# Kernel optimization log

Hardware: AMD Instinct MI355X
Metric: run time of the kernel (lower is better)

Reference implementation:

```python
import jax, jax.numpy as jnp
import numpy as np

B, L, D_MODEL = 8, 2048, 768
D_INNER, D_STATE, DT_RANK, K = 1536, 16, 48, 4


def setup_inputs() -> dict:
    key = jax.random.key(0)
    ks = jax.random.split(key, 9)
    s = 0.02
    return {
        "hidden_states": jax.random.normal(ks[0], (B, L, D_MODEL), jnp.float32),
        "W_in": jax.random.normal(ks[1], (D_MODEL, 2 * D_INNER), jnp.float32) * s,
        "conv_w": jax.random.normal(ks[2], (D_INNER, 1, K), jnp.float32) * s,
        "conv_b": jax.random.normal(ks[3], (D_INNER,), jnp.float32) * s,
        "W_x": jax.random.normal(ks[4], (DT_RANK + 2 * D_STATE, D_INNER), jnp.float32) * s,
        "W_dt": jax.random.normal(ks[5], (D_INNER, DT_RANK), jnp.float32) * s,
        "b_dt": jax.random.normal(ks[6], (D_INNER,), jnp.float32) * s,
        "A_log": jax.random.normal(ks[7], (D_INNER, D_STATE), jnp.float32),
        "D_param": jax.random.normal(ks[8], (D_INNER,), jnp.float32),
    }


def _mamba(hidden_states, W_in, conv_w, conv_b, W_x, W_dt, b_dt, A_log, D_param):
    # in_proj then chunk into ssm branch (x) and gating residual (res)
    xz = hidden_states @ W_in                      # (B, L, 2*d_inner)
    x, res = jnp.split(xz, 2, axis=-1)             # each (B, L, d_inner)

    # causal depthwise conv over time, then SiLU
    xc = x.transpose(0, 2, 1)                      # (B, C, L)
    xc = jax.lax.conv_general_dilated(
        xc, conv_w, window_strides=(1,), padding=[(K - 1, 0)],
        feature_group_count=D_INNER, dimension_numbers=("NCH", "OIH", "NCH"))
    x = jax.nn.silu(xc + conv_b[None, :, None]).transpose(0, 2, 1)  # (B, L, d_inner)

    # input-dependent SSM parameters
    x_dbl = x @ W_x.T                              # (B, L, dt_rank + 2*d_state)
    dt = jax.nn.softplus(x_dbl[..., :DT_RANK] @ W_dt.T + b_dt)      # (B, L, d_inner)
    Bm = x_dbl[..., DT_RANK:DT_RANK + D_STATE]     # (B, L, d_state)
    Cm = x_dbl[..., DT_RANK + D_STATE:]            # (B, L, d_state)
    A = -jnp.exp(A_log)                            # (d_inner, d_state)

    def step(h, inp):
        x_t, dt_t, B_t, C_t = inp                  # (B,d_inner),(B,d_inner),(B,d_state),(B,d_state)
        dA = jnp.exp(dt_t[..., None] * A)          # (B, d_inner, d_state)
        dBx = (dt_t * x_t)[..., None] * B_t[:, None, :]
        h = dA * h + dBx
        y = jnp.einsum("bds,bs->bd", h, C_t)
        return h, y

    xs = (x.transpose(1, 0, 2), dt.transpose(1, 0, 2),
          Bm.transpose(1, 0, 2), Cm.transpose(1, 0, 2))
    h0 = jnp.zeros((x.shape[0], D_INNER, D_STATE), x.dtype)
    _, ys = jax.lax.scan(step, h0, xs)             # ys: (L, B, d_inner)
    y = ys.transpose(1, 0, 2) + x * D_param        # skip term
    return y * jax.nn.silu(res)                    # gated output (B, L, d_inner)


def reference(hidden_states, W_in, conv_w, conv_b, W_x, W_dt, b_dt, A_log, D_param):
    return _mamba(hidden_states, W_in, conv_w, conv_b, W_x, W_dt, b_dt, A_log, D_param)
```

## Files before the change

kernel.cpp:

```cpp
#include <hip/hip_runtime.h>
#include <hip/hip_bf16.h>
#include <stdint.h>

#define B_SZ 8
#define L_SZ 2048
#define DM 768
#define DI 1536
#define DS 16
#define DR 48
#define M_SZ (B_SZ * L_SZ)
#define N1 (2 * DI)

#define NC 32
#define TC (L_SZ / NC)
#define CH (B_SZ * DI)
#define KS 6
#define NT (DM / 64)
#define L2E 1.44269504088896f

typedef short short8 __attribute__((ext_vector_type(8)));
typedef float f32x4 __attribute__((ext_vector_type(4)));

__device__ __forceinline__ ushort f2b(float f) {
  __hip_bfloat16 h = __float2bfloat16(f);
  return *reinterpret_cast<ushort*>(&h);
}
__device__ __forceinline__ float b2f(ushort u) {
  __hip_bfloat16 h;
  *reinterpret_cast<ushort*>(&h) = u;
  return __bfloat162float(h);
}
__device__ __forceinline__ ushort f2h(float f) {
  _Float16 h = (_Float16)f;
  return *reinterpret_cast<ushort*>(&h);
}
__device__ __forceinline__ float h2f(ushort u) {
  _Float16 h;
  *reinterpret_cast<ushort*>(&h) = u;
  return (float)h;
}

__device__ __forceinline__ void gl16(const ushort* g, ushort* l) {
  __builtin_amdgcn_global_load_lds(
      (const __attribute__((address_space(1))) void*)g,
      (__attribute__((address_space(3))) void*)l, 16, 0, 0);
}

#define EXP4(dst, src)                                      \
  {                                                         \
    float _e0, _e1, _e2, _e3;                               \
    asm("v_exp_f32 %0, %1" : "=v"(_e0) : "v"((src)[0]));    \
    asm("v_exp_f32 %0, %1" : "=v"(_e1) : "v"((src)[1]));    \
    asm("v_exp_f32 %0, %1" : "=v"(_e2) : "v"((src)[2]));    \
    asm("v_exp_f32 %0, %1" : "=v"(_e3) : "v"((src)[3]));    \
    (dst) = f32x4{_e0, _e1, _e2, _e3};                      \
  }


__global__ __launch_bounds__(256) void prep_all(const float4* __restrict__ hs4,
                                                const float* __restrict__ w_in,
                                                const float* __restrict__ wx_f,
                                                const float* __restrict__ wdt_f,
                                                ushort4* __restrict__ A1,
                                                ushort* __restrict__ wt,
                                                ushort* __restrict__ wx_b,
                                                ushort* __restrict__ wdt_p) {
  const int n4 = M_SZ * DM / 4;
  const int nT = 3072 * 96;
  const int nwx = 80 * DI;
  const int nwdt = DI * 64;
  int idx = blockIdx.x * 256 + threadIdx.x;
  if (idx < n4) {
    float4 v = hs4[idx];
    ushort4 o;
    o.x = f2b(v.x); o.y = f2b(v.y); o.z = f2b(v.z); o.w = f2b(v.w);
    A1[idx] = o;
  } else if (idx < n4 + nT) {
    int j = idx - n4;
    int n = j % 3072;
    int kb = (j / 3072) * 8;
    short8 o;
#pragma unroll
    for (int q = 0; q < 8; ++q) o[q] = (short)f2b(w_in[(size_t)(kb + q) * 3072 + n]);
    *(short8*)(wt + (size_t)n * DM + kb) = o;
  } else if (idx < n4 + nT + nwx) {
    int j = idx - n4 - nT;
    wx_b[j] = f2b(wx_f[j]);
  } else if (idx < n4 + nT + nwx + nwdt) {
    int j = idx - n4 - nT - nwx;
    int col = j >> 6, k = j & 63;
    wdt_p[j] = (k < DR) ? f2b(wdt_f[col * DR + k]) : (ushort)0;
  }
}


__global__ __launch_bounds__(512, 1) void gemm_xz(const ushort* __restrict__ A,
                                                  const ushort* __restrict__ Bt,
                                                  ushort* __restrict__ xout,
                                                  ushort* __restrict__ gateout) {
  __shared__ ushort lds[65536];

  const int t = threadIdx.x;
  const int lane = t & 63;
  const int wid = t >> 6;
  const int wm = wid >> 2, wn = wid & 3;
  const int r = lane & 15, hi = lane >> 4;

  const int g = blockIdx.x;
  const int swz = (g & 7) * (768 / 8) + (g >> 3);
  const int bx = swz & 63;
  const int by = swz >> 6;
  const int bm = bx * 256;
  const int bn = by * 256;

  const bool isA = wid < 4;
  const int w4 = wid & 3;
  const ushort* gsrc[8];
  int ldso[8];
#pragma unroll
  for (int i = 0; i < 8; ++i) {
    int c = w4 * 8 + i;
    int mg = c >> 1, kkc = c & 1;
    gsrc[i] = (isA ? A + (size_t)(bm + mg * 16 + r) * DM
                   : Bt + (size_t)(bn + mg * 16 + r) * DM) + kkc * 32 + hi * 8;
    ldso[i] = (isA ? 0 : 16384) + c * 512;
  }

  f32x4 acc[8][4];
#pragma unroll
  for (int m = 0; m < 8; ++m)
#pragma unroll
    for (int n = 0; n < 4; ++n) acc[m][n] = f32x4{0.f, 0.f, 0.f, 0.f};

#pragma unroll
  for (int i = 0; i < 8; ++i) gl16(gsrc[i], &lds[ldso[i]]);
  asm volatile("s_waitcnt vmcnt(0)" ::: "memory");
  __builtin_amdgcn_s_barrier();

  for (int kt = 0; kt < NT; ++kt) {
    const int cur = kt & 1;
    const ushort* bufA = &lds[cur * 32768];
    const ushort* bufB = bufA + 16384;
    ushort* nxt = &lds[(cur ^ 1) * 32768];
    const int koff = (kt + 1) * 64;
    const bool more = (kt + 1 < NT);

    short8 afr[4][2], bfr[2][2];
#pragma unroll
    for (int q = 0; q < 4; ++q) {
      const int mq = q >> 1, nq = q & 1;
      if (nq == 0) {
#pragma unroll
        for (int m = 0; m < 4; ++m)
#pragma unroll
          for (int kk = 0; kk < 2; ++kk)
            afr[m][kk] = *(const short8*)&bufA[((wm * 8 + mq * 4 + m) * 2 + kk) * 512 + lane * 8];
      }
#pragma unroll
      for (int n = 0; n < 2; ++n)
#pragma unroll
        for (int kk = 0; kk < 2; ++kk)
          bfr[n][kk] = *(const short8*)&bufB[((wn * 4 + nq * 2 + n) * 2 + kk) * 512 + lane * 8];

      if (q == 0 && more) {
#pragma unroll
        for (int i = 0; i < 8; ++i) gl16(gsrc[i] + koff, nxt + ldso[i]);
      }

      asm volatile("s_barrier" ::: "memory");

      __builtin_amdgcn_s_setprio(1);
#pragma unroll
      for (int m = 0; m < 4; ++m)
#pragma unroll
        for (int n = 0; n < 2; ++n) {
          f32x4 a = acc[mq * 4 + m][nq * 2 + n];
          a = __builtin_amdgcn_mfma_f32_16x16x32_bf16(afr[m][0], bfr[n][0], a, 0, 0, 0);
          a = __builtin_amdgcn_mfma_f32_16x16x32_bf16(afr[m][1], bfr[n][1], a, 0, 0, 0);
          acc[mq * 4 + m][nq * 2 + n] = a;
        }
      __builtin_amdgcn_s_setprio(0);

      if (q == 3) asm volatile("s_waitcnt vmcnt(0)" ::: "memory");
      asm volatile("s_barrier" ::: "memory");
    }
  }

  const bool isx = (bn < DI);
  ushort* outp = isx ? xout : gateout;
  const int cbase = bn - (isx ? 0 : DI) + wn * 64;
#pragma unroll
  for (int mf = 0; mf < 8; ++mf)
#pragma unroll
    for (int nf = 0; nf < 4; ++nf) {
      int col = cbase + nf * 16 + r;
#pragma unroll
      for (int j = 0; j < 4; ++j) {
        int row = bm + wm * 128 + mf * 16 + hi * 4 + j;
        float v = acc[mf][nf][j];
        if (!isx) v = v / (1.f + __expf(-v));
        outp[(size_t)row * DI + col] = f2b(v);
      }
    }
}


__global__ __launch_bounds__(256) void conv_silu(const ushort* __restrict__ xp,
                                                 const float* __restrict__ cw,
                                                 const float* __restrict__ cb,
                                                 ushort* __restrict__ xc) {
  int tid = blockIdx.x * 256 + threadIdx.x;
  const int nd = DI / 8;
  int db = tid % nd;
  int row = tid / nd;
  int d0 = db * 8;
  int l = row & (L_SZ - 1);
  const ushort* base = xp + (size_t)row * DI + d0;
  short8 z8 = {0, 0, 0, 0, 0, 0, 0, 0};
  short8 x0 = *(const short8*)base;
  short8 xm1 = (l >= 1) ? *(const short8*)(base - DI) : z8;
  short8 xm2 = (l >= 2) ? *(const short8*)(base - 2 * DI) : z8;
  short8 xm3 = (l >= 3) ? *(const short8*)(base - 3 * DI) : z8;
  short8 o;
#pragma unroll
  for (int j = 0; j < 8; ++j) {
    float4 w = *(const float4*)(cw + (size_t)(d0 + j) * 4);
    float a = cb[d0 + j] + w.x * b2f((ushort)xm3[j]) + w.y * b2f((ushort)xm2[j]) +
              w.z * b2f((ushort)xm1[j]) + w.w * b2f((ushort)x0[j]);
    float s = a / (1.f + __expf(-a));
    o[j] = (short)f2b(s);
  }
  *(short8*)(xc + (size_t)row * DI + d0) = o;
}


__global__ __launch_bounds__(256) void xdbl_gemm(const ushort* __restrict__ xc,
                                                 const ushort* __restrict__ wx,
                                                 float* __restrict__ xdp) {
  int wave = blockIdx.x * 4 + (threadIdx.x >> 6);
  int ks = blockIdx.y;
  int lane = threadIdx.x & 63;
  int r = lane & 15, hi = lane >> 4;
  int row0 = wave * 16;
  f32x4 acc[5];
#pragma unroll
  for (int n = 0; n < 5; ++n) acc[n] = f32x4{0.f, 0.f, 0.f, 0.f};
  const int kbeg = ks * (DI / KS), kend = kbeg + DI / KS;
  for (int k0 = kbeg; k0 < kend; k0 += 32) {
    short8 a = *(const short8*)(xc + (size_t)(row0 + r) * DI + k0 + hi * 8);
#pragma unroll
    for (int n = 0; n < 5; ++n) {
      short8 b = *(const short8*)(wx + (size_t)(n * 16 + r) * DI + k0 + hi * 8);
      acc[n] = __builtin_amdgcn_mfma_f32_16x16x32_bf16(a, b, acc[n], 0, 0, 0);
    }
  }
  float* op = xdp + (size_t)ks * M_SZ * 80;
#pragma unroll
  for (int n = 0; n < 5; ++n)
#pragma unroll
    for (int j = 0; j < 4; ++j)
      op[(size_t)(row0 + hi * 4 + j) * 80 + n * 16 + r] = acc[n][j];
}

__global__ __launch_bounds__(256) void reduce_xd(const float4* __restrict__ xdp,
                                                 float4* __restrict__ xd) {
  int i = blockIdx.x * 256 + threadIdx.x;
  if (i >= M_SZ * 20) return;
  float4 s = xdp[i];
#pragma unroll
  for (int k = 1; k < KS; ++k) {
    float4 v = xdp[(size_t)k * M_SZ * 20 + i];
    s.x += v.x; s.y += v.y; s.z += v.z; s.w += v.w;
  }
  xd[i] = s;
}


__device__ __forceinline__ short8 pack8f(const float* p) {
  short8 v;
#pragma unroll
  for (int i = 0; i < 8; ++i) v[i] = (short)f2b(p[i]);
  return v;
}

__global__ __launch_bounds__(256) void dt_gemm(const float* __restrict__ xd,
                                               const ushort* __restrict__ wdtp,
                                               const float* __restrict__ bdt,
                                               ushort* __restrict__ dt) {
  int wave = blockIdx.x * 4 + (threadIdx.x >> 6);
  int lane = threadIdx.x & 63;
  int r = lane & 15, hi = lane >> 4;
  int row0 = wave * 16;
  int c0 = blockIdx.y * 64;

  float atmp[8];
  const float* ap = xd + (size_t)(row0 + r) * 80 + hi * 8;
  float4 q0 = *(const float4*)ap, q1 = *(const float4*)(ap + 4);
  atmp[0] = q0.x; atmp[1] = q0.y; atmp[2] = q0.z; atmp[3] = q0.w;
  atmp[4] = q1.x; atmp[5] = q1.y; atmp[6] = q1.z; atmp[7] = q1.w;
  short8 a0 = pack8f(atmp);
  short8 a1 = {0, 0, 0, 0, 0, 0, 0, 0};
  if (hi < 2) {
    const float* ap1 = xd + (size_t)(row0 + r) * 80 + 32 + hi * 8;
    float4 p0 = *(const float4*)ap1, p1 = *(const float4*)(ap1 + 4);
    atmp[0] = p0.x; atmp[1] = p0.y; atmp[2] = p0.z; atmp[3] = p0.w;
    atmp[4] = p1.x; atmp[5] = p1.y; atmp[6] = p1.z; atmp[7] = p1.w;
    a1 = pack8f(atmp);
  }

  f32x4 acc[4];
#pragma unroll
  for (int n = 0; n < 4; ++n) acc[n] = f32x4{0.f, 0.f, 0.f, 0.f};
#pragma unroll
  for (int n = 0; n < 4; ++n) {
    const ushort* wp = wdtp + (size_t)(c0 + n * 16 + r) * 64;
    short8 b0 = *(const short8*)(wp + hi * 8);
    short8 b1 = *(const short8*)(wp + 32 + hi * 8);
    acc[n] = __builtin_amdgcn_mfma_f32_16x16x32_bf16(a0, b0, acc[n], 0, 0, 0);
    acc[n] = __builtin_amdgcn_mfma_f32_16x16x32_bf16(a1, b1, acc[n], 0, 0, 0);
  }
#pragma unroll
  for (int n = 0; n < 4; ++n)
#pragma unroll
    for (int j = 0; j < 4; ++j) {
      int col = c0 + n * 16 + r;
      float z = acc[n][j] + bdt[col];
      float sp = (z > 20.f) ? z : __logf(1.f + __expf(z));
      dt[(size_t)(row0 + hi * 4 + j) * DI + col] = f2h(sp);
    }
}


__global__ __launch_bounds__(256) void scan_pass1(const ushort* __restrict__ dt,
                                                  const ushort* __restrict__ xc,
                                                  const float* __restrict__ xd,
                                                  const float* __restrict__ A_log,
                                                  float* __restrict__ hend,
                                                  float* __restrict__ sumdt) {
  const int d = blockIdx.x * 256 + threadIdx.x;
  const int c = blockIdx.y, b = blockIdx.z;
  const int t0 = c * TC;

  __shared__ float Bs[TC * 16];
  for (int i = threadIdx.x; i < TC * 16; i += 256) {
    int tt = i >> 4, s = i & 15;
    Bs[i] = xd[((size_t)(b * L_SZ + t0 + tt)) * 80 + DR + s];
  }

  f32x4 a4[4];
  const float4* al4 = (const float4*)(A_log + (size_t)d * DS);
#pragma unroll
  for (int q = 0; q < 4; ++q) {
    float4 v = al4[q];
    a4[q] = f32x4{-__expf(v.x) * L2E, -__expf(v.y) * L2E,
                  -__expf(v.z) * L2E, -__expf(v.w) * L2E};
  }

  __syncthreads();

  f32x4 h4[4];
#pragma unroll
  for (int q = 0; q < 4; ++q) h4[q] = f32x4{0.f, 0.f, 0.f, 0.f};
  float sd = 0.f;

  const ushort* dtp = dt + ((size_t)b * L_SZ + t0) * DI + d;
  const ushort* xp = xc + ((size_t)b * L_SZ + t0) * DI + d;

  ushort dtu_n = *dtp;
  ushort xu_n = *xp;
  const f32x4* bp4 = (const f32x4*)Bs;
  for (int tt = 0; tt < TC; ++tt) {
    dtp += DI; xp += DI;
    ushort dtu = dtu_n;
    ushort xu = xu_n;
    dtu_n = *dtp;
    xu_n = *xp;
    float dtv = h2f(dtu);
    float xv = b2f(xu);
    sd += dtv;
    float dx = dtv * xv;
    f32x4 dts = f32x4{dtv, dtv, dtv, dtv};
    f32x4 dxs = f32x4{dx, dx, dx, dx};
#pragma unroll
    for (int q = 0; q < 4; ++q) {
      f32x4 arg = dts * a4[q];
      f32x4 dA;
      EXP4(dA, arg);
      h4[q] = dA * h4[q] + dxs * bp4[q];
    }
    bp4 += 4;
  }

  const size_t ch = (size_t)b * DI + d;
  sumdt[ch * NC + c] = sd;
  f32x4* hp = (f32x4*)&hend[((size_t)c * CH + ch) * 16];
#pragma unroll
  for (int q = 0; q < 4; ++q) hp[q] = h4[q];
}

__global__ __launch_bounds__(256) void scan_pass2(const float* __restrict__ A_log,
                                                  const float* __restrict__ sumdt,
                                                  const float* __restrict__ hend,
                                                  float* __restrict__ hstart) {
  int idx = blockIdx.x * 256 + threadIdx.x;
  int ch = idx >> 4, s = idx & 15;
  int d = ch % DI;
  float A = -__expf(A_log[d * DS + s]);
  float h = 0.f;
  for (int c = 0; c < NC; ++c) {
    hstart[((size_t)c * CH + ch) * 16 + s] = h;
    float sd = sumdt[(size_t)ch * NC + c];
    h = __expf(A * sd) * h + hend[((size_t)c * CH + ch) * 16 + s];
  }
}

__global__ __launch_bounds__(256) void scan_pass3(const ushort* __restrict__ dt,
                                                  const ushort* __restrict__ xc,
                                                  const float* __restrict__ xd,
                                                  const ushort* __restrict__ gateb,
                                                  const float* __restrict__ A_log,
                                                  const float* __restrict__ Dp,
                                                  const float* __restrict__ hstart,
                                                  float* __restrict__ out) {
  const int d = blockIdx.x * 256 + threadIdx.x;
  const int c = blockIdx.y, b = blockIdx.z;
  const int t0 = c * TC;

  __shared__ float Bs[TC * 16];
  __shared__ float Cs[TC * 16];
  for (int i = threadIdx.x; i < TC * 16; i += 256) {
    int tt = i >> 4, s = i & 15;
    size_t row = ((size_t)(b * L_SZ + t0 + tt)) * 80;
    Bs[i] = xd[row + DR + s];
    Cs[i] = xd[row + DR + DS + s];
  }

  f32x4 a4[4];
  const float4* al4 = (const float4*)(A_log + (size_t)d * DS);
#pragma unroll
  for (int q = 0; q < 4; ++q) {
    float4 v = al4[q];
    a4[q] = f32x4{-__expf(v.x) * L2E, -__expf(v.y) * L2E,
                  -__expf(v.z) * L2E, -__expf(v.w) * L2E};
  }
  const float Dpv = Dp[d];

  const size_t ch = (size_t)b * DI + d;
  f32x4 h4[4];
  const f32x4* hp = (const f32x4*)&hstart[((size_t)c * CH + ch) * 16];
#pragma unroll
  for (int q = 0; q < 4; ++q) h4[q] = hp[q];

  __syncthreads();

  const ushort* dtp = dt + ((size_t)b * L_SZ + t0) * DI + d;
  const ushort* xp = xc + ((size_t)b * L_SZ + t0) * DI + d;
  const ushort* gp = gateb + ((size_t)b * L_SZ + t0) * DI + d;
  float* op = out + ((size_t)b * L_SZ + t0) * DI + d;

  ushort dtu_n = *dtp;
  ushort xu_n = *xp;
  ushort gu_n = *gp;
  const f32x4* bp4 = (const f32x4*)Bs;
  const f32x4* cp4 = (const f32x4*)Cs;
  for (int tt = 0; tt < TC; ++tt) {
    dtp += DI; xp += DI; gp += DI;
    ushort dtu = dtu_n;
    ushort xu = xu_n;
    ushort gu = gu_n;
    dtu_n = *dtp;
    xu_n = *xp;
    gu_n = *gp;
    float dtv = h2f(dtu);
    float xv = b2f(xu);
    float gv = b2f(gu);
    float dx = dtv * xv;
    f32x4 dts = f32x4{dtv, dtv, dtv, dtv};
    f32x4 dxs = f32x4{dx, dx, dx, dx};
    f32x4 y4 = f32x4{0.f, 0.f, 0.f, 0.f};
#pragma unroll
    for (int q = 0; q < 4; ++q) {
      f32x4 arg = dts * a4[q];
      f32x4 dA;
      EXP4(dA, arg);
      h4[q] = dA * h4[q] + dxs * bp4[q];
      y4 = y4 + h4[q] * cp4[q];
    }
    bp4 += 4; cp4 += 4;
    float y = (y4[0] + y4[1]) + (y4[2] + y4[3]);
    op[0] = (y + xv * Dpv) * gv;
    op += DI;
  }
}


extern "C" void kernel_launch(void* const* d_in, const int* in_sizes, int n_in,
                              void* d_out, int out_size, void* d_ws, size_t ws_size,
                              hipStream_t stream) {
  const float* hs     = (const float*)d_in[0];
  const float* W_in   = (const float*)d_in[1];
  const float* conv_w = (const float*)d_in[2];
  const float* conv_b = (const float*)d_in[3];
  const float* W_x    = (const float*)d_in[4];
  const float* W_dt   = (const float*)d_in[5];
  const float* b_dt   = (const float*)d_in[6];
  const float* A_log  = (const float*)d_in[7];
  const float* D_par  = (const float*)d_in[8];
  float* out = (float*)d_out;
  char* ws = (char*)d_ws;

  size_t o = 0;
  ushort* A1   = (ushort*)(ws + o); o += (size_t)M_SZ * DM * 2;
  ushort* Wt1  = (ushort*)(ws + o); o += (size_t)N1 * DM * 2;
  ushort* xpre = (ushort*)(ws + o); o += (size_t)M_SZ * DI * 2;
  ushort* gate = (ushort*)(ws + o); o += (size_t)M_SZ * DI * 2;
  ushort* xcv  = (ushort*)(ws + o); o += (size_t)M_SZ * DI * 2;
  float*  xdbl = (float*)(ws + o);  o += (size_t)M_SZ * 80 * 4;
  ushort* dtb  = (ushort*)(ws + o); o += (size_t)M_SZ * DI * 2;
  float*  xdp  = (float*)(ws + o);  o += (size_t)KS * M_SZ * 80 * 4;
  ushort* Wxb  = (ushort*)(ws + o); o += (size_t)80 * DI * 2;
  ushort* Wdtp = (ushort*)(ws + o); o += (size_t)DI * 64 * 2;
  if (ws_size < o) return;

  float* hend   = (float*)(ws + 0);
  float* hstart = (float*)(ws + (size_t)NC * CH * 16 * 4);
  float* sumdt  = (float*)(ws + (size_t)2 * NC * CH * 16 * 4);

  const int nprep = M_SZ * DM / 4 + 3072 * 96 + 80 * DI + DI * 64;
  prep_all<<<dim3((nprep + 255) / 256), dim3(256), 0, stream>>>(
      (const float4*)hs, W_in, W_x, W_dt, (ushort4*)A1, Wt1, Wxb, Wdtp);

  gemm_xz<<<dim3((M_SZ / 256) * (N1 / 256)), dim3(512), 0, stream>>>(A1, Wt1, xpre, gate);

  conv_silu<<<dim3(M_SZ * DI / 8 / 256), dim3(256), 0, stream>>>(xpre, conv_w, conv_b, xcv);

  xdbl_gemm<<<dim3(M_SZ / 64, KS), dim3(256), 0, stream>>>(xcv, Wxb, xdp);
  reduce_xd<<<dim3((M_SZ * 20 + 255) / 256), dim3(256), 0, stream>>>((const float4*)xdp, (float4*)xdbl);

  dt_gemm<<<dim3(M_SZ / 64, 24), dim3(256), 0, stream>>>(xdbl, Wdtp, b_dt, dtb);

  scan_pass1<<<dim3(DI / 256, NC, B_SZ), dim3(256), 0, stream>>>(dtb, xcv, xdbl, A_log, hend, sumdt);
  scan_pass2<<<dim3(CH * 16 / 256), dim3(256), 0, stream>>>(A_log, sumdt, hend, hstart);
  scan_pass3<<<dim3(DI / 256, NC, B_SZ), dim3(256), 0, stream>>>(dtb, xcv, xdbl, gate,
                                                                 A_log, D_par, hstart, out);
}
```

Baseline: 438.2 us.

## Switch in_proj GEMM to triple-buffered K=32 pipeline with rotating LDS buffers

Restructures the xz projection GEMM main loop from double-buffered 64-wide K tiles to triple-buffered 32-wide K tiles, prefetching two stages ahead with rotating LDS buffer pointers. Each wave now loads four 16-row slices per stage, and waits use vmcnt(4) so one stage of loads can remain in flight while computing. The goal is better overlap of global loads with MFMA work and a smaller LDS footprint. In exchange there are more loop iterations and barriers per unit of K, which could add synchronization overhead.

```diff
diff --git a/kernel.cpp b/kernel.cpp
--- a/kernel.cpp
+++ b/kernel.cpp
@@ -15,7 +15,7 @@
 #define TC (L_SZ / NC)
 #define CH (B_SZ * DI)
 #define KS 6
-#define NT (DM / 64)
+#define NT2 (DM / 32)
 #define L2E 1.44269504088896f
 
 typedef short short8 __attribute__((ext_vector_type(8)));
@@ -98,7 +98,7 @@
                                                   const ushort* __restrict__ Bt,
                                                   ushort* __restrict__ xout,
                                                   ushort* __restrict__ gateout) {
-  __shared__ ushort lds[65536];
+  __shared__ ushort lds[49152];
 
   const int t = threadIdx.x;
   const int lane = t & 63;
@@ -113,17 +113,16 @@
   const int bm = bx * 256;
   const int bn = by * 256;
 
-  const bool isA = wid < 4;
-  const int w4 = wid & 3;
-  const ushort* gsrc[8];
-  int ldso[8];
-#pragma unroll
-  for (int i = 0; i < 8; ++i) {
-    int c = w4 * 8 + i;
-    int mg = c >> 1, kkc = c & 1;
-    gsrc[i] = (isA ? A + (size_t)(bm + mg * 16 + r) * DM
-                   : Bt + (size_t)(bn + mg * 16 + r) * DM) + kkc * 32 + hi * 8;
-    ldso[i] = (isA ? 0 : 16384) + c * 512;
+  const ushort* gsrc[4];
+  int ldso[4];
+#pragma unroll
+  for (int i = 0; i < 4; ++i) {
+    int c = wid * 4 + i;
+    if (c < 16)
+      gsrc[i] = A + (size_t)(bm + c * 16 + r) * DM + hi * 8;
+    else
+      gsrc[i] = Bt + (size_t)(bn + (c - 16) * 16 + r) * DM + hi * 8;
+    ldso[i] = c * 512;
   }
 
   f32x4 acc[8][4];
@@ -132,58 +131,59 @@
 #pragma unroll
     for (int n = 0; n < 4; ++n) acc[m][n] = f32x4{0.f, 0.f, 0.f, 0.f};
 
-#pragma unroll
-  for (int i = 0; i < 8; ++i) gl16(gsrc[i], &lds[ldso[i]]);
-  asm volatile("s_waitcnt vmcnt(0)" ::: "memory");
+  ushort* b0 = lds;
+  ushort* b1 = lds + 16384;
+  ushort* b2 = lds + 32768;
+
+#pragma unroll
+  for (int i = 0; i < 4; ++i) gl16(gsrc[i], b0 + ldso[i]);
+#pragma unroll
+  for (int i = 0; i < 4; ++i) gl16(gsrc[i] + 32, b1 + ldso[i]);
+  asm volatile("s_waitcnt vmcnt(4)" ::: "memory");
   __builtin_amdgcn_s_barrier();
 
-  for (int kt = 0; kt < NT; ++kt) {
-    const int cur = kt & 1;
-    const ushort* bufA = &lds[cur * 32768];
-    const ushort* bufB = bufA + 16384;
-    ushort* nxt = &lds[(cur ^ 1) * 32768];
-    const int koff = (kt + 1) * 64;
-    const bool more = (kt + 1 < NT);
-
-    short8 afr[4][2], bfr[2][2];
-#pragma unroll
-    for (int q = 0; q < 4; ++q) {
-      const int mq = q >> 1, nq = q & 1;
-      if (nq == 0) {
-#pragma unroll
-        for (int m = 0; m < 4; ++m)
-#pragma unroll
-          for (int kk = 0; kk < 2; ++kk)
-            afr[m][kk] = *(const short8*)&bufA[((wm * 8 + mq * 4 + m) * 2 + kk) * 512 + lane * 8];
+  for (int kt = 0; kt < NT2; ++kt) {
+    const bool stage = (kt + 2 < NT2);
+    const int koff = (kt + 2) * 32;
+
+    short8 bfr[4];
+#pragma unroll
+    for (int n = 0; n < 4; ++n)
+      bfr[n] = *(const short8*)&b0[(16 + wn * 4 + n) * 512 + lane * 8];
+
+#pragma unroll
+    for (int q = 0; q < 2; ++q) {
+      short8 afr[4];
+#pragma unroll
+      for (int m = 0; m < 4; ++m)
+        afr[m] = *(const short8*)&b0[(wm * 8 + q * 4 + m) * 512 + lane * 8];
+
+      if (stage) {
+        gl16(gsrc[2 * q] + koff, b2 + ldso[2 * q]);
+        gl16(gsrc[2 * q + 1] + koff, b2 + ldso[2 * q + 1]);
       }
-#pragma unroll
-      for (int n = 0; n < 2; ++n)
-#pragma unroll
-        for (int kk = 0; kk < 2; ++kk)
-          bfr[n][kk] = *(const short8*)&bufB[((wn * 4 + nq * 2 + n) * 2 + kk) * 512 + lane * 8];
-
-      if (q == 0 && more) {
-#pragma unroll
-        for (int i = 0; i < 8; ++i) gl16(gsrc[i] + koff, nxt + ldso[i]);
+
+      asm volatile("s_barrier" ::: "memory");
+
+      __builtin_amdgcn_s_setprio(1);
+#pragma unroll
+      for (int m = 0; m < 4; ++m)
+#pragma unroll
+        for (int n = 0; n < 4; ++n)
+          acc[q * 4 + m][n] =
+              __builtin_amdgcn_mfma_f32_16x16x32_bf16(afr[m], bfr[n], acc[q * 4 + m][n], 0, 0, 0);
+      __builtin_amdgcn_s_setprio(0);
+
+      if (q == 1) {
+        if (stage)
+          asm volatile("s_waitcnt vmcnt(4)" ::: "memory");
+        else
+          asm volatile("s_waitcnt vmcnt(0)" ::: "memory");
       }
-
-      asm volatile("s_barrier" ::: "memory");
-
-      __builtin_amdgcn_s_setprio(1);
-#pragma unroll
-      for (int m = 0; m < 4; ++m)
-#pragma unroll
-        for (int n = 0; n < 2; ++n) {
-          f32x4 a = acc[mq * 4 + m][nq * 2 + n];
-          a = __builtin_amdgcn_mfma_f32_16x16x32_bf16(afr[m][0], bfr[n][0], a, 0, 0, 0);
-          a = __builtin_amdgcn_mfma_f32_16x16x32_bf16(afr[m][1], bfr[n][1], a, 0, 0, 0);
-          acc[mq * 4 + m][nq * 2 + n] = a;
-        }
-      __builtin_amdgcn_s_setprio(0);
-
-      if (q == 3) asm volatile("s_waitcnt vmcnt(0)" ::: "memory");
       asm volatile("s_barrier" ::: "memory");
     }
+
+    ushort* tmp = b0; b0 = b1; b1 = b2; b2 = tmp;
   }
 
   const bool isx = (bn < DI);
```

After: 421.0 us. 3.9% less time.
